# Kernel optimization log

Measured on AMD Instinct MI355X. Metric: run time of the kernel, lower is better.

## Reference

```python
import jax, jax.numpy as jnp
import numpy as np

FORGET_RADIX = 10
HIDDEN_RADIX = 23
LN2 = float(np.log(2.0))
MAX_FORGET = 0.875
BATCH, IN_SIZE, H_SIZE = 8192, 1024, 2048
G = H_SIZE // 2  # group size (h_size // 2)


def setup_inputs() -> dict:
    key = jax.random.key(0)
    ks = jax.random.split(key, 6)
    x = jax.random.normal(ks[0], (BATCH, IN_SIZE), dtype=jnp.float32)
    # hidden is a fixed-point (radix 23) int state; values correspond to floats in (-0.125, 0.125)
    hidden = jax.random.randint(ks[1], (BATCH, H_SIZE), -(2**20), 2**20, dtype=jnp.int32)

    def lin(k, fan_in, fan_out):
        kw, kb = jax.random.split(k)
        s = 1.0 / np.sqrt(fan_in)
        W = jax.random.uniform(kw, (fan_in, fan_out), jnp.float32, -s, s)
        b = jax.random.uniform(kb, (fan_out,), jnp.float32, -s, s)
        return W, b

    W_zr1, b_zr1 = lin(ks[2], IN_SIZE + G, H_SIZE)
    W_g1, b_g1 = lin(ks[3], IN_SIZE + G, G)
    W_zr2, b_zr2 = lin(ks[4], IN_SIZE + G, H_SIZE)
    W_g2, b_g2 = lin(ks[5], IN_SIZE + G, G)
    return {"x": x, "hidden": hidden,
            "W_zr1": W_zr1, "b_zr1": b_zr1, "W_g1": W_g1, "b_g1": b_g1,
            "W_zr2": W_zr2, "b_zr2": b_zr2, "W_g2": W_g2, "b_g2": b_g2,
            "slice_dim": 0}


def _to_float(h_fix, radix):
    # ConvertToFloat: fixed-point int -> float
    return h_fix.astype(jnp.float32) / np.float32(2.0 ** radix)


def _to_fixed(v, radix):
    # ConvertToFixed: float -> fixed-point int (truncation toward zero, like Tensor.int())
    return jnp.trunc(v * np.float32(2.0 ** radix)).astype(jnp.int64)


def reference(x, hidden, W_zr1, b_zr1, W_g1, b_g1, W_zr2, b_zr2, W_g2, b_g2, slice_dim):
    h = hidden.astype(jnp.int64)  # widen so h * z_fix (up to ~2^34) does not overflow
    h1, h2 = h[:, :G], h[:, G:]

    # ---- group 1 update (reads h2) ----
    h2_fl = _to_float(h2, HIDDEN_RADIX)
    zr1 = jax.nn.sigmoid(jnp.concatenate([x, h2_fl], axis=1) @ W_zr1 + b_zr1)
    z1, r1 = zr1[:, :G], zr1[:, G:]
    z1 = MAX_FORGET * z1 + (1.0 - MAX_FORGET)
    g1 = jnp.tanh(jnp.concatenate([x, r1 * h2_fl], axis=1) @ W_g1 + b_g1)
    z1_fix = jnp.maximum(_to_fixed(z1, FORGET_RADIX), 1)  # EnsureNotForgetAll
    h1 = jnp.floor_divide(h1 * z1_fix, 2 ** FORGET_RADIX)  # FixedMultiply, buf=None, mask=1
    h1 = h1 + _to_fixed((1.0 - z1) * g1, HIDDEN_RADIX)     # + MaskFixedMultiply(update1, 1)

    # ---- group 2 update (reads updated h1) ----
    h1_fl = _to_float(h1, HIDDEN_RADIX)
    zr2 = jax.nn.sigmoid(jnp.concatenate([x, h1_fl], axis=1) @ W_zr2 + b_zr2)
    z2, r2 = zr2[:, :G], zr2[:, G:]
    z2 = MAX_FORGET * z2 + (1.0 - MAX_FORGET)
    g2 = jnp.tanh(jnp.concatenate([x, r2 * h1_fl], axis=1) @ W_g2 + b_g2)
    z2_fix = jnp.maximum(_to_fixed(z2, FORGET_RADIX), 1)
    h2 = jnp.floor_divide(h2 * z2_fix, 2 ** FORGET_RADIX)
    h2 = h2 + _to_fixed((1.0 - z2) * g2, HIDDEN_RADIX)

    recurrent_hidden = jnp.concatenate([h1, h2], axis=1).astype(jnp.int32)
    output_hidden = recurrent_hidden.astype(jnp.float32) / np.float32(2.0 ** HIDDEN_RADIX)

    optimal_bits = (jnp.sum(-jnp.log(z1[:, slice_dim:]) / LN2)
                    + jnp.sum(-jnp.log(z2) / LN2)
                    + 32.0 * slice_dim * x.shape[0])
    return recurrent_hidden, output_hidden, optimal_bits
```

## Files before the change

### kernel.cpp

```cpp
#include <hip/hip_runtime.h>
#include <hip/hip_bf16.h>

#define BATCH   8192
#define IN_SZ   1024
#define HSZ     2048
#define GG      1024
#define KTOT    2048

typedef __hip_bfloat16 bf16;
typedef __attribute__((ext_vector_type(8))) short  short8;
typedef __attribute__((ext_vector_type(4))) short  short4e;
typedef __attribute__((ext_vector_type(4))) float  floatx4;

typedef __attribute__((address_space(1))) const void gvoid_t;
typedef __attribute__((address_space(3))) void       lvoid_t;

__device__ __forceinline__ void async_ld16(void* lds, const void* g) {
  __builtin_amdgcn_global_load_lds((gvoid_t*)g, (lvoid_t*)lds, 16, 0, 0);
}

__global__ void prep_all(const float* __restrict__ x, bf16* __restrict__ xb,
                         const int* __restrict__ hidden, bf16* __restrict__ hf,
                         float* accp,
                         const float* __restrict__ W_zr1, const float* __restrict__ W_g1,
                         const float* __restrict__ W_zr2, const float* __restrict__ W_g2,
                         bf16* __restrict__ wt_zr1, bf16* __restrict__ wt_g1,
                         bf16* __restrict__ wt_zr2, bf16* __restrict__ wt_g2) {
  int b = blockIdx.x;
  int t = threadIdx.x;
  if (b < 3072) {
    const float* W; bf16* Wt; int N; int tb = b;
    if (tb < 1024)      { W = W_zr1; Wt = wt_zr1; N = 2048; }
    else if (tb < 1536) { W = W_g1;  Wt = wt_g1;  N = 1024; tb -= 1024; }
    else if (tb < 2560) { W = W_zr2; Wt = wt_zr2; N = 2048; tb -= 1536; }
    else                { W = W_g2;  Wt = wt_g2;  N = 1024; tb -= 2560; }
    int ntn = N >> 6;
    int k0 = (tb / ntn) * 64, n0 = (tb % ntn) * 64;
    __shared__ float tile[64][65];
    int kk = t >> 4, nn = (t & 15) * 4;
#pragma unroll
    for (int s = 0; s < 4; ++s) {
      int row = kk + s * 16;
      float4 v = *(const float4*)&W[(size_t)(k0 + row) * N + n0 + nn];
      tile[row][nn + 0] = v.x; tile[row][nn + 1] = v.y;
      tile[row][nn + 2] = v.z; tile[row][nn + 3] = v.w;
    }
    __syncthreads();
    int k8 = (t & 7) * 8;
#pragma unroll
    for (int s = 0; s < 2; ++s) {
      int nl = (t >> 3) + s * 32;
      bf16 vals[8];
#pragma unroll
      for (int u = 0; u < 8; ++u) vals[u] = __float2bfloat16(tile[k8 + u][nl]);
      *(short8*)&Wt[(size_t)(n0 + nl) * KTOT + k0 + k8] = *(short8*)vals;
    }
  } else {
    int idx = (b - 3072) * 256 + t;
    int i = idx * 4;
    float4 xv = *(const float4*)(x + i);
    xb[i + 0] = __float2bfloat16(xv.x);
    xb[i + 1] = __float2bfloat16(xv.y);
    xb[i + 2] = __float2bfloat16(xv.z);
    xb[i + 3] = __float2bfloat16(xv.w);
    int m = i >> 10, j = i & 1023;
    int4 hv = *(const int4*)(hidden + m * HSZ + GG + j);
    const float sc = 1.0f / 8388608.0f;
    hf[i + 0] = __float2bfloat16((float)hv.x * sc);
    hf[i + 1] = __float2bfloat16((float)hv.y * sc);
    hf[i + 2] = __float2bfloat16((float)hv.z * sc);
    hf[i + 3] = __float2bfloat16((float)hv.w * sc);
    if (idx == 0) *accp = 0.0f;
  }
}


#define BAR() asm volatile("s_barrier" ::: "memory")

#define DS_A(buf, qm) do {                                                   \
  _Pragma("unroll") for (int ii = 0; ii < 4; ++ii) {                         \
    const bf16* _ap = As + (buf)*16384 + (wm*128 + (qm)*64 + ii*16 + r16)*64;\
    af[ii][0] = *(const short8*)(const void*)(_ap + pcq0);                   \
    af[ii][1] = *(const short8*)(const void*)(_ap + pcq1);                   \
  } } while (0)

#define DS_B(buf, qn) do {                                                   \
  _Pragma("unroll") for (int jj = 0; jj < NJQ; ++jj) {                       \
    const int _brow = (BN == 256) ? (wn*64 + (qn)*32 + jj*16 + r16)          \
                                  : (wn*32 + (qn)*16 + r16);                 \
    const bf16* _bp = Bs + (buf)*BSTR + _brow*64;                            \
    bfr[jj][0] = *(const short8*)(const void*)(_bp + pcq0);                  \
    bfr[jj][1] = *(const short8*)(const void*)(_bp + pcq1);                  \
  } } while (0)

#define MFMA_Q(qm, qn) do {                                                  \
  _Pragma("unroll") for (int ii = 0; ii < 4; ++ii)                           \
  _Pragma("unroll") for (int jj = 0; jj < NJQ; ++jj) {                       \
    floatx4& _c = acc[(qm)*4 + ii][(qn)*NJQ + jj];                           \
    _c = __builtin_amdgcn_mfma_f32_16x16x32_bf16(af[ii][0], bfr[jj][0], _c, 0, 0, 0); \
    _c = __builtin_amdgcn_mfma_f32_16x16x32_bf16(af[ii][1], bfr[jj][1], _c, 0, 0, 0); \
  } } while (0)

#define STAGE_A(buf, qm, tk) do {                                            \
  const int _t = (tk);                                                       \
  const bf16* _p = (_t < 16 ? A0 : A1);                                      \
  const int _k = ((_t & 15) << 6) + gch8;                                    \
  async_ld16(As + (buf)*16384 + (qm)*4096 + w*512 + lnoff,        _p + a_sro[qm][0] + _k); \
  async_ld16(As + (buf)*16384 + 8192 + (qm)*4096 + w*512 + lnoff, _p + a_sro[qm][1] + _k); \
} while (0)

#define STAGE_B(buf, qn, tk) do {                                            \
  const int _k = ((tk) << 6) + gch8;                                         \
  if constexpr (BN == 256) {                                                 \
    async_ld16(Bs + (buf)*BSTR + ((w>>2)*64 + (qn)*32 + (w&3)*8)*64 + lnoff,       Bt + b_sro[qn][0] + _k); \
    async_ld16(Bs + (buf)*BSTR + (128 + (w>>2)*64 + (qn)*32 + (w&3)*8)*64 + lnoff, Bt + b_sro[qn][1] + _k); \
  } else {                                                                   \
    async_ld16(Bs + (buf)*BSTR + ((w>>1)*32 + (qn)*16 + (w&1)*8)*64 + lnoff,       Bt + b_sro[qn][0] + _k); \
  }                                                                          \
} while (0)

#define PHASE(buf, qm, qn, NEWA, STAGE_STMT, DOVM) do {                      \
  if (NEWA) DS_A(buf, qm);                                                   \
  DS_B(buf, qn);                                                             \
  STAGE_STMT;                                                                \
  BAR();                                                                     \
  asm volatile("s_waitcnt lgkmcnt(0)" ::: "memory");                         \
  __builtin_amdgcn_sched_barrier(0);                                         \
  __builtin_amdgcn_s_setprio(1);                                             \
  MFMA_Q(qm, qn);                                                            \
  __builtin_amdgcn_s_setprio(0);                                             \
  if (DOVM) { if constexpr (BN == 256) asm volatile("s_waitcnt vmcnt(4)" ::: "memory"); \
              else                     asm volatile("s_waitcnt vmcnt(3)" ::: "memory"); } \
  BAR();                                                                     \
} while (0)

template<int BN>
__device__ __forceinline__ void mainloop8(const bf16* __restrict__ A0,
                                          const bf16* __restrict__ A1,
                                          const bf16* __restrict__ Bt,
                                          bf16* As, bf16* Bs,
                                          int m0, int n0,
                                          floatx4 (&acc)[8][BN / 64]) {
  constexpr int NJQ  = BN / 128;
  constexpr int BSTR = BN * 64;
  const int t    = threadIdx.x;
  const int lane = t & 63;
  const int w    = t >> 6;
  const int l3   = lane >> 3;
  const int gch8 = (((lane & 7) ^ l3) << 3);
  const int lnoff = lane << 3;
  const int wm = w & 1, wn = w >> 1;
  const int q = lane >> 4, r16 = lane & 15;
  const int pcq0 = ((q)     ^ (r16 & 7)) << 3;
  const int pcq1 = ((4 + q) ^ (r16 & 7)) << 3;

  int a_sro[2][2], b_sro[2][2];
#pragma unroll
  for (int qm = 0; qm < 2; ++qm)
#pragma unroll
    for (int h = 0; h < 2; ++h)
      a_sro[qm][h] = (m0 + h*128 + qm*64 + w*8 + l3) * 1024;
#pragma unroll
  for (int qn = 0; qn < 2; ++qn) {
    if constexpr (BN == 256) {
#pragma unroll
      for (int h = 0; h < 2; ++h)
        b_sro[qn][h] = (n0 + h*128 + (w>>2)*64 + qn*32 + (w&3)*8 + l3) * KTOT;
    } else {
      b_sro[qn][0] = (n0 + (w>>1)*32 + qn*16 + (w&1)*8 + l3) * KTOT;
      b_sro[qn][1] = 0;
    }
  }

  STAGE_A(0, 0, 0); STAGE_B(0, 0, 0);
  STAGE_A(0, 1, 0); STAGE_B(0, 1, 0);
  STAGE_A(1, 0, 1); STAGE_B(1, 0, 1);
  if constexpr (BN == 256) asm volatile("s_waitcnt vmcnt(4)" ::: "memory");
  else                     asm volatile("s_waitcnt vmcnt(3)" ::: "memory");
  BAR();

#pragma unroll 1
  for (int it = 0; it < KTOT / 128; ++it) {
    const int tO = 2*it + 1;
    const int t2 = (2*it + 2 < KTOT/64) ? (2*it + 2) : (KTOT/64 - 1);
    const int t3 = (2*it + 3 < KTOT/64) ? (2*it + 3) : (KTOT/64 - 1);
    short8 af[4][2];
    short8 bfr[NJQ][2];
    PHASE(0, 0, 0, 1, STAGE_A(1, 1, tO), 0);
    PHASE(0, 0, 1, 0, STAGE_B(1, 1, tO), 0);
    PHASE(0, 1, 0, 1, STAGE_A(0, 0, t2), 0);
    PHASE(0, 1, 1, 0, STAGE_B(0, 0, t2), 1);
    PHASE(1, 0, 0, 1, STAGE_A(0, 1, t2), 0);
    PHASE(1, 0, 1, 0, STAGE_B(0, 1, t2), 0);
    PHASE(1, 1, 0, 1, STAGE_A(1, 0, t3), 0);
    PHASE(1, 1, 1, 0, STAGE_B(1, 0, t3), 1);
  }
  asm volatile("s_waitcnt vmcnt(0)" ::: "memory");
  __syncthreads();
}

__global__ void __launch_bounds__(512, 2)
gemm_zr8(const bf16* __restrict__ xb, const bf16* __restrict__ hfp,
         const bf16* __restrict__ Bt, const float* __restrict__ bias,
         bf16* __restrict__ zbuf, bf16* __restrict__ rh,
         const int* __restrict__ slice_ptr, int use_slice,
         float* __restrict__ accp) {
  __shared__ __attribute__((aligned(16))) char smem[131072];
  bf16* As = (bf16*)smem;
  bf16* Bs = (bf16*)(smem + 65536);
  const int m0 = blockIdx.y * 256;
  const int n0 = blockIdx.x * 256;
  floatx4 acc[8][4];
#pragma unroll
  for (int i = 0; i < 8; ++i)
#pragma unroll
    for (int j = 0; j < 4; ++j) acc[i][j] = (floatx4)0.0f;

  mainloop8<256>(xb, hfp, Bt, As, Bs, m0, n0, acc);

  const int t = threadIdx.x;
  const int lane = t & 63, w = t >> 6;
  const int wm = w & 1, wn = w >> 1;
  const int q = lane >> 4, r16 = lane & 15;
  float* lds_f = (float*)smem;
  const bool zmode = (n0 < GG);
  const int nmin = use_slice ? *slice_ptr : 0;
  float bn[4];
#pragma unroll
  for (int j = 0; j < 4; ++j) bn[j] = bias[n0 + wn*64 + j*16 + r16];
  float lsum = 0.0f;

#pragma unroll
  for (int p = 0; p < 2; ++p) {
#pragma unroll
    for (int i4 = 0; i4 < 4; ++i4)
#pragma unroll
      for (int j = 0; j < 4; ++j) {
        const int n_loc = wn*64 + j*16 + r16;
        const int n = n0 + n_loc;
#pragma unroll
        for (int rr = 0; rr < 4; ++rr) {
          const int lr = wm*64 + i4*16 + q*4 + rr;
          float v = acc[p*4 + i4][j][rr] + bn[j];
          float s = 1.0f / (1.0f + __expf(-v));
          float ov;
          if (zmode) {
            float z = 0.875f * s + 0.125f;
            if (n >= nmin) lsum += -__log2f(z);
            ov = z;
          } else {
            ov = s;
          }
          lds_f[lr*256 + ((((n_loc >> 2) ^ (lr & 7)) << 2) | (n_loc & 3))] = ov;
        }
      }
    __syncthreads();
#pragma unroll
    for (int s2 = 0; s2 < 16; ++s2) {
      const int r = w*16 + s2;
      const int c = lane;
      floatx4 v4 = *(const floatx4*)&lds_f[r*256 + ((c ^ (r & 7)) << 2)];
      const int m = m0 + (r >> 6)*128 + p*64 + (r & 63);
      const int ncol = n0 + c*4;
      if (zmode) {
        bf16 o[4];
#pragma unroll
        for (int e = 0; e < 4; ++e) o[e] = __float2bfloat16(v4[e]);
        *(short4e*)&zbuf[(size_t)m * GG + ncol] = *(short4e*)o;
      } else {
        const int jc = ncol - GG;
        short4e hv = *(const short4e*)&hfp[(size_t)m * GG + jc];
        bf16 o[4];
#pragma unroll
        for (int e = 0; e < 4; ++e) {
          float hfv = __uint_as_float((unsigned)(unsigned short)hv[e] << 16);
          o[e] = __float2bfloat16(v4[e] * hfv);
        }
        *(short4e*)&rh[(size_t)m * GG + jc] = *(short4e*)o;
      }
    }
    __syncthreads();
  }
#pragma unroll
  for (int off = 32; off > 0; off >>= 1) lsum += __shfl_down(lsum, off, 64);
  float* sf = (float*)smem;
  if (lane == 0) sf[w] = lsum;
  __syncthreads();
  if (t == 0)
    atomicAdd(accp, sf[0]+sf[1]+sf[2]+sf[3]+sf[4]+sf[5]+sf[6]+sf[7]);
}

__global__ void __launch_bounds__(512, 2)
gemm_g8(const bf16* __restrict__ xb, const bf16* __restrict__ rh,
        const bf16* __restrict__ Bt, const float* __restrict__ bias,
        const bf16* __restrict__ zbuf, const int* __restrict__ hidden,
        int col_off,
        float* __restrict__ out0, float* __restrict__ out1,
        bf16* __restrict__ hf_out, int write_hf,
        int write_bits, const float* __restrict__ accp,
        const int* __restrict__ slice_ptr, float* __restrict__ out2) {
  __shared__ __attribute__((aligned(16))) char smem[131072];
  bf16* As = (bf16*)smem;
  bf16* Bs = (bf16*)(smem + 65536);
  const int m0 = blockIdx.y * 256;
  const int n0 = blockIdx.x * 128;
  floatx4 acc[8][2];
#pragma unroll
  for (int i = 0; i < 8; ++i)
#pragma unroll
    for (int j = 0; j < 2; ++j) acc[i][j] = (floatx4)0.0f;

  mainloop8<128>(xb, rh, Bt, As, Bs, m0, n0, acc);

  const int t = threadIdx.x;
  const int lane = t & 63, w = t >> 6;
  const int wm = w & 1, wn = w >> 1;
  const int q = lane >> 4, r16 = lane & 15;
  float* lds_f = (float*)smem;
  float bn[2];
#pragma unroll
  for (int j = 0; j < 2; ++j) bn[j] = bias[n0 + wn*32 + j*16 + r16];

#pragma unroll
  for (int i = 0; i < 8; ++i)
#pragma unroll
    for (int j = 0; j < 2; ++j) {
      const int n_loc = wn*32 + j*16 + r16;
#pragma unroll
      for (int rr = 0; rr < 4; ++rr) {
        const int lr = wm*128 + i*16 + q*4 + rr;
        lds_f[lr*128 + ((((n_loc >> 2) ^ (lr & 7)) << 2) | (n_loc & 3))] =
            acc[i][j][rr] + bn[j];
      }
    }
  __syncthreads();
#pragma unroll
  for (int s2 = 0; s2 < 16; ++s2) {
    const int r = w*2 + (lane >> 5) + s2*16;
    const int c = lane & 31;
    floatx4 v4 = *(const floatx4*)&lds_f[r*128 + ((c ^ (r & 7)) << 2)];
    const int m = m0 + r;
    const int ncol = n0 + c*4;
    short4e zb = *(const short4e*)&zbuf[(size_t)m * GG + ncol];
    int4 hd = *(const int4*)&hidden[(size_t)m * HSZ + col_off + ncol];
    const int hvv[4] = {hd.x, hd.y, hd.z, hd.w};
    floatx4 w0, w1;
    bf16 ob[4];
#pragma unroll
    for (int e = 0; e < 4; ++e) {
      float v = v4[e];
      float ex = __expf(2.0f * v);
      float gg = 1.0f - 2.0f / (ex + 1.0f);
      float z = __uint_as_float((unsigned)(unsigned short)zb[e] << 16);
      int zfix = (int)(z * 1024.0f);
      if (zfix < 1) zfix = 1;
      long long h = hvv[e];
      long long hupd = (h * (long long)zfix) >> 10;
      float t2f = (1.0f - z) * gg * 8388608.0f;
      long long f2 = (long long)t2f;
      int hnew = (int)(hupd + f2);
      w0[e] = (float)hnew;
      w1[e] = (float)hnew * (1.0f / 8388608.0f);
      ob[e] = __float2bfloat16(w1[e]);
    }
    const size_t ob_ = (size_t)m * HSZ + col_off + ncol;
    *(floatx4*)&out0[ob_] = w0;
    *(floatx4*)&out1[ob_] = w1;
    if (write_hf) *(short4e*)&hf_out[(size_t)m * GG + ncol] = *(short4e*)ob;
  }
  if (write_bits && blockIdx.x == 0 && blockIdx.y == 0 && t == 0)
    *out2 = *accp + 32.0f * (float)(*slice_ptr) * (float)BATCH;
}

extern "C" void kernel_launch(void* const* d_in, const int* in_sizes, int n_in,
                              void* d_out, int out_size, void* d_ws, size_t ws_size,
                              hipStream_t stream) {
  const float* x      = (const float*)d_in[0];
  const int*   hidden = (const int*)d_in[1];
  const float* W_zr1  = (const float*)d_in[2];
  const float* b_zr1  = (const float*)d_in[3];
  const float* W_g1   = (const float*)d_in[4];
  const float* b_g1   = (const float*)d_in[5];
  const float* W_zr2  = (const float*)d_in[6];
  const float* b_zr2  = (const float*)d_in[7];
  const float* W_g2   = (const float*)d_in[8];
  const float* b_g2   = (const float*)d_in[9];
  const int*   slice  = (const int*)d_in[10];

  char* ws = (char*)d_ws;
  size_t off = 0;
  auto alloc = [&](size_t bytes) -> void* {
    void* p = ws + off;
    off += (bytes + 255) & ~(size_t)255;
    return p;
  };
  bf16* xb     = (bf16*)alloc((size_t)BATCH * IN_SZ * 2);
  bf16* wt_zr1 = (bf16*)alloc((size_t)2048 * 2048 * 2);
  bf16* wt_g1  = (bf16*)alloc((size_t)1024 * 2048 * 2);
  bf16* wt_zr2 = (bf16*)alloc((size_t)2048 * 2048 * 2);
  bf16* wt_g2  = (bf16*)alloc((size_t)1024 * 2048 * 2);
  bf16* hf     = (bf16*)alloc((size_t)BATCH * GG * 2);
  bf16* rh     = (bf16*)alloc((size_t)BATCH * GG * 2);
  bf16* zbuf   = (bf16*)alloc((size_t)BATCH * GG * 2);
  float* accp  = (float*)alloc(256);

  float* out0 = (float*)d_out;
  float* out1 = out0 + (size_t)BATCH * HSZ;
  float* out2 = out0 + 2 * (size_t)BATCH * HSZ;

  prep_all<<<3072 + 8192, 256, 0, stream>>>(x, xb, hidden, hf, accp,
                                            W_zr1, W_g1, W_zr2, W_g2,
                                            wt_zr1, wt_g1, wt_zr2, wt_g2);

  gemm_zr8<<<dim3(8, 32), 512, 0, stream>>>(xb, hf, wt_zr1, b_zr1, zbuf, rh, slice, 1, accp);
  gemm_g8<<<dim3(8, 32), 512, 0, stream>>>(xb, rh, wt_g1, b_g1, zbuf, hidden, 0,
                                           out0, out1, hf, 1, 0, accp, slice, out2);
  gemm_zr8<<<dim3(8, 32), 512, 0, stream>>>(xb, hf, wt_zr2, b_zr2, zbuf, rh, slice, 0, accp);
  gemm_g8<<<dim3(8, 32), 512, 0, stream>>>(xb, rh, wt_g2, b_g2, zbuf, hidden, 1024,
                                           out0, out1, hf, 0, 1, accp, slice, out2);
}
```

Baseline: 528.3 us.

## Double-buffer register fragments and remap g-GEMM warps to a 4x2 layout

Replaces the shared templated main loop with separate zr and g main loops. Each loop ping-pongs A/B register fragments so the LDS reads for the next quarter-tile are issued before the MFMAs of the current one, waiting with partial lgkmcnt instead of draining to zero. The g GEMM also changes its warp tiling from 2x4 to 4x2 with 64-wide N per warp, and its B staging and epilogue indexing change to match. This adds register pressure and depends on tricky hand-tuned vmcnt and lgkmcnt counts, which risks stalls or races if they are wrong.

```diff
diff --git a/kernel.cpp b/kernel.cpp
--- a/kernel.cpp
+++ b/kernel.cpp
@@ -75,83 +75,50 @@
 }
 
 
-#define BAR() asm volatile("s_barrier" ::: "memory")
-
-#define DS_A(buf, qm) do {                                                   \
-  _Pragma("unroll") for (int ii = 0; ii < 4; ++ii) {                         \
-    const bf16* _ap = As + (buf)*16384 + (wm*128 + (qm)*64 + ii*16 + r16)*64;\
-    af[ii][0] = *(const short8*)(const void*)(_ap + pcq0);                   \
-    af[ii][1] = *(const short8*)(const void*)(_ap + pcq1);                   \
-  } } while (0)
-
-#define DS_B(buf, qn) do {                                                   \
-  _Pragma("unroll") for (int jj = 0; jj < NJQ; ++jj) {                       \
-    const int _brow = (BN == 256) ? (wn*64 + (qn)*32 + jj*16 + r16)          \
-                                  : (wn*32 + (qn)*16 + r16);                 \
-    const bf16* _bp = Bs + (buf)*BSTR + _brow*64;                            \
-    bfr[jj][0] = *(const short8*)(const void*)(_bp + pcq0);                  \
-    bfr[jj][1] = *(const short8*)(const void*)(_bp + pcq1);                  \
-  } } while (0)
-
-#define MFMA_Q(qm, qn) do {                                                  \
-  _Pragma("unroll") for (int ii = 0; ii < 4; ++ii)                           \
-  _Pragma("unroll") for (int jj = 0; jj < NJQ; ++jj) {                       \
-    floatx4& _c = acc[(qm)*4 + ii][(qn)*NJQ + jj];                           \
-    _c = __builtin_amdgcn_mfma_f32_16x16x32_bf16(af[ii][0], bfr[jj][0], _c, 0, 0, 0); \
-    _c = __builtin_amdgcn_mfma_f32_16x16x32_bf16(af[ii][1], bfr[jj][1], _c, 0, 0, 0); \
-  } } while (0)
-
-#define STAGE_A(buf, qm, tk) do {                                            \
-  const int _t = (tk);                                                       \
-  const bf16* _p = (_t < 16 ? A0 : A1);                                      \
-  const int _k = ((_t & 15) << 6) + gch8;                                    \
-  async_ld16(As + (buf)*16384 + (qm)*4096 + w*512 + lnoff,        _p + a_sro[qm][0] + _k); \
-  async_ld16(As + (buf)*16384 + 8192 + (qm)*4096 + w*512 + lnoff, _p + a_sro[qm][1] + _k); \
-} while (0)
-
-#define STAGE_B(buf, qn, tk) do {                                            \
-  const int _k = ((tk) << 6) + gch8;                                         \
-  if constexpr (BN == 256) {                                                 \
-    async_ld16(Bs + (buf)*BSTR + ((w>>2)*64 + (qn)*32 + (w&3)*8)*64 + lnoff,       Bt + b_sro[qn][0] + _k); \
-    async_ld16(Bs + (buf)*BSTR + (128 + (w>>2)*64 + (qn)*32 + (w&3)*8)*64 + lnoff, Bt + b_sro[qn][1] + _k); \
-  } else {                                                                   \
-    async_ld16(Bs + (buf)*BSTR + ((w>>1)*32 + (qn)*16 + (w&1)*8)*64 + lnoff,       Bt + b_sro[qn][0] + _k); \
-  }                                                                          \
-} while (0)
-
-#define PHASE(buf, qm, qn, NEWA, STAGE_STMT, DOVM) do {                      \
-  if (NEWA) DS_A(buf, qm);                                                   \
-  DS_B(buf, qn);                                                             \
-  STAGE_STMT;                                                                \
-  BAR();                                                                     \
-  asm volatile("s_waitcnt lgkmcnt(0)" ::: "memory");                         \
-  __builtin_amdgcn_sched_barrier(0);                                         \
-  __builtin_amdgcn_s_setprio(1);                                             \
-  MFMA_Q(qm, qn);                                                            \
-  __builtin_amdgcn_s_setprio(0);                                             \
-  if (DOVM) { if constexpr (BN == 256) asm volatile("s_waitcnt vmcnt(4)" ::: "memory"); \
-              else                     asm volatile("s_waitcnt vmcnt(3)" ::: "memory"); } \
-  BAR();                                                                     \
-} while (0)
-
-template<int BN>
-__device__ __forceinline__ void mainloop8(const bf16* __restrict__ A0,
-                                          const bf16* __restrict__ A1,
-                                          const bf16* __restrict__ Bt,
-                                          bf16* As, bf16* Bs,
-                                          int m0, int n0,
-                                          floatx4 (&acc)[8][BN / 64]) {
-  constexpr int NJQ  = BN / 128;
-  constexpr int BSTR = BN * 64;
-  const int t    = threadIdx.x;
-  const int lane = t & 63;
-  const int w    = t >> 6;
-  const int l3   = lane >> 3;
+#define BAR()        asm volatile("s_barrier" ::: "memory")
+#define WAIT_VM(n)   asm volatile("s_waitcnt vmcnt(" #n ")" ::: "memory")
+#define WAIT_LG(n)   asm volatile("s_waitcnt lgkmcnt(" #n ")" ::: "memory")
+#define SCHED0       __builtin_amdgcn_sched_barrier(0)
+#define PRIO1        __builtin_amdgcn_s_setprio(1)
+#define PRIO0        __builtin_amdgcn_s_setprio(0)
+
+#define ZR_SA(buf, qm, tk) { const int _kt = (tk) * 64; const bf16* _p; int _kl; \
+  if (_kt < IN_SZ) { _p = A0g; _kl = _kt; } else { _p = A1g; _kl = _kt - IN_SZ; } \
+  async_ld16(As + (buf)*16384 + (qm)*4096 + w*512 + lnoff,        _p + a_sro[qm][0] + _kl + gch8); \
+  async_ld16(As + (buf)*16384 + 8192 + (qm)*4096 + w*512 + lnoff, _p + a_sro[qm][1] + _kl + gch8); }
+
+#define ZR_SB(buf, qn, tk) { const int _k = (tk) * 64 + gch8; \
+  async_ld16(Bs + (buf)*16384 + ((w>>2)*64 + (qn)*32 + (w&3)*8)*64 + lnoff,       Btg + b_sro[qn][0] + _k); \
+  async_ld16(Bs + (buf)*16384 + (128 + (w>>2)*64 + (qn)*32 + (w&3)*8)*64 + lnoff, Btg + b_sro[qn][1] + _k); }
+
+#define ZR_RDA(dst, buf, qm) { _Pragma("unroll") for (int ii = 0; ii < 4; ++ii) { \
+  const bf16* _ap = As + (buf)*16384 + (wm*128 + (qm)*64 + ii*16 + r16)*64; \
+  dst[ii][0] = *(const short8*)(const void*)(_ap + pcq0); \
+  dst[ii][1] = *(const short8*)(const void*)(_ap + pcq1); } }
+
+#define ZR_RDB(dst, buf, qn) { _Pragma("unroll") for (int jj = 0; jj < 2; ++jj) { \
+  const bf16* _bp = Bs + (buf)*16384 + (wn*64 + (qn)*32 + jj*16 + r16)*64; \
+  dst[jj][0] = *(const short8*)(const void*)(_bp + pcq0); \
+  dst[jj][1] = *(const short8*)(const void*)(_bp + pcq1); } }
+
+#define ZR_MF(qm, qn, AF, BF) { _Pragma("unroll") for (int ii = 0; ii < 4; ++ii) \
+  _Pragma("unroll") for (int jj = 0; jj < 2; ++jj) { \
+    floatx4& _c = acc[(qm)*4 + ii][(qn)*2 + jj]; \
+    _c = __builtin_amdgcn_mfma_f32_16x16x32_bf16(AF[ii][0], BF[jj][0], _c, 0, 0, 0); \
+    _c = __builtin_amdgcn_mfma_f32_16x16x32_bf16(AF[ii][1], BF[jj][1], _c, 0, 0, 0); } }
+
+__device__ __forceinline__ void mainloop_zr(const bf16* __restrict__ A0g,
+                                            const bf16* __restrict__ A1g,
+                                            const bf16* __restrict__ Btg,
+                                            bf16* As, bf16* Bs,
+                                            int m0, int n0, floatx4 (&acc)[8][4]) {
+  const int t = threadIdx.x, lane = t & 63, w = t >> 6;
+  const int l3 = lane >> 3;
   const int gch8 = (((lane & 7) ^ l3) << 3);
   const int lnoff = lane << 3;
   const int wm = w & 1, wn = w >> 1;
   const int q = lane >> 4, r16 = lane & 15;
-  const int pcq0 = ((q)     ^ (r16 & 7)) << 3;
+  const int pcq0 = ((q) ^ (r16 & 7)) << 3;
   const int pcq1 = ((4 + q) ^ (r16 & 7)) << 3;
 
   int a_sro[2][2], b_sro[2][2];
@@ -159,41 +126,109 @@
   for (int qm = 0; qm < 2; ++qm)
 #pragma unroll
     for (int h = 0; h < 2; ++h)
-      a_sro[qm][h] = (m0 + h*128 + qm*64 + w*8 + l3) * 1024;
-#pragma unroll
-  for (int qn = 0; qn < 2; ++qn) {
-    if constexpr (BN == 256) {
-#pragma unroll
-      for (int h = 0; h < 2; ++h)
-        b_sro[qn][h] = (n0 + h*128 + (w>>2)*64 + qn*32 + (w&3)*8 + l3) * KTOT;
-    } else {
-      b_sro[qn][0] = (n0 + (w>>1)*32 + qn*16 + (w&1)*8 + l3) * KTOT;
-      b_sro[qn][1] = 0;
-    }
-  }
-
-  STAGE_A(0, 0, 0); STAGE_B(0, 0, 0);
-  STAGE_A(0, 1, 0); STAGE_B(0, 1, 0);
-  STAGE_A(1, 0, 1); STAGE_B(1, 0, 1);
-  if constexpr (BN == 256) asm volatile("s_waitcnt vmcnt(4)" ::: "memory");
-  else                     asm volatile("s_waitcnt vmcnt(3)" ::: "memory");
+      a_sro[qm][h] = (m0 + h*128 + qm*64 + w*8 + l3) * IN_SZ;
+#pragma unroll
+  for (int qn = 0; qn < 2; ++qn)
+#pragma unroll
+    for (int h = 0; h < 2; ++h)
+      b_sro[qn][h] = (n0 + h*128 + (w>>2)*64 + qn*32 + (w&3)*8 + l3) * KTOT;
+
+  short8 afA[4][2], afB[4][2], bfrA[2][2], bfrB[2][2];
+
+  ZR_SA(0,0,0); ZR_SB(0,0,0); ZR_SB(0,1,0); ZR_SA(0,1,0);
+  ZR_SA(1,0,1); ZR_SB(1,0,1); ZR_SB(1,1,1); ZR_SA(1,1,1);
+  WAIT_VM(10);
+  BAR();
+  ZR_RDA(afA, 0, 0);
+  ZR_RDB(bfrA, 0, 0);
+  WAIT_LG(0);
   BAR();
 
 #pragma unroll 1
   for (int it = 0; it < KTOT / 128; ++it) {
-    const int tO = 2*it + 1;
-    const int t2 = (2*it + 2 < KTOT/64) ? (2*it + 2) : (KTOT/64 - 1);
-    const int t3 = (2*it + 3 < KTOT/64) ? (2*it + 3) : (KTOT/64 - 1);
-    short8 af[4][2];
-    short8 bfr[NJQ][2];
-    PHASE(0, 0, 0, 1, STAGE_A(1, 1, tO), 0);
-    PHASE(0, 0, 1, 0, STAGE_B(1, 1, tO), 0);
-    PHASE(0, 1, 0, 1, STAGE_A(0, 0, t2), 0);
-    PHASE(0, 1, 1, 0, STAGE_B(0, 0, t2), 1);
-    PHASE(1, 0, 0, 1, STAGE_A(0, 1, t2), 0);
-    PHASE(1, 0, 1, 0, STAGE_B(0, 1, t2), 0);
-    PHASE(1, 1, 0, 1, STAGE_A(1, 0, t3), 0);
-    PHASE(1, 1, 1, 0, STAGE_B(1, 0, t3), 1);
+    const int tn0 = (2*it + 2 < KTOT/64) ? (2*it + 2) : (KTOT/64 - 1);
+    const int tn1 = (2*it + 3 < KTOT/64) ? (2*it + 3) : (KTOT/64 - 1);
+    ZR_RDB(bfrB,0,1); ZR_SA(0,0,tn0); BAR(); WAIT_LG(4);  SCHED0; PRIO1; ZR_MF(0,0,afA,bfrA); PRIO0; WAIT_VM(10); BAR();
+    ZR_RDA(afB,0,1);  ZR_SB(0,0,tn0); BAR(); WAIT_LG(8);  SCHED0; PRIO1; ZR_MF(0,1,afA,bfrB); PRIO0; WAIT_VM(10); BAR();
+    ZR_RDA(afA,1,0);  ZR_SB(0,1,tn0); BAR(); WAIT_LG(8);  SCHED0; PRIO1; ZR_MF(1,0,afB,bfrA); PRIO0; WAIT_VM(10); BAR();
+    ZR_RDB(bfrA,1,0); ZR_SA(0,1,tn0); BAR(); WAIT_LG(4);  SCHED0; PRIO1; ZR_MF(1,1,afB,bfrB); PRIO0; WAIT_VM(10); BAR();
+    ZR_RDB(bfrB,1,1); ZR_SA(1,0,tn1); BAR(); WAIT_LG(4);  SCHED0; PRIO1; ZR_MF(0,0,afA,bfrA); PRIO0; WAIT_VM(10); BAR();
+    ZR_RDA(afB,1,1);  ZR_SB(1,0,tn1); BAR(); WAIT_LG(8);  SCHED0; PRIO1; ZR_MF(0,1,afA,bfrB); PRIO0; WAIT_VM(10); BAR();
+    ZR_RDA(afA,0,0);  ZR_SB(1,1,tn1); BAR(); WAIT_LG(8);  SCHED0; PRIO1; ZR_MF(1,0,afB,bfrA); PRIO0; WAIT_VM(10); BAR();
+    ZR_RDB(bfrA,0,0); ZR_SA(1,1,tn1); BAR(); WAIT_LG(4);  SCHED0; PRIO1; ZR_MF(1,1,afB,bfrB); PRIO0; WAIT_VM(10); BAR();
+  }
+  asm volatile("s_waitcnt vmcnt(0)" ::: "memory");
+  __syncthreads();
+}
+
+#define G_SB(buf, tk) { const int _k = (tk) * 64 + gch8; \
+  async_ld16(Bs + (buf)*8192 + w*512 + lnoff,        Btg + b_srg[0] + _k); \
+  async_ld16(Bs + (buf)*8192 + 4096 + w*512 + lnoff, Btg + b_srg[1] + _k); }
+
+#define G_RDA(dst, buf, qm) { _Pragma("unroll") for (int ii = 0; ii < 2; ++ii) { \
+  const bf16* _ap = As + (buf)*16384 + (mwb + (qm)*64 + ii*16 + r16)*64; \
+  dst[ii][0] = *(const short8*)(const void*)(_ap + pcq0); \
+  dst[ii][1] = *(const short8*)(const void*)(_ap + pcq1); } }
+
+#define G_RDB(dst, buf, qn) { _Pragma("unroll") for (int jj = 0; jj < 2; ++jj) { \
+  const bf16* _bp = Bs + (buf)*8192 + (nw*64 + (qn)*32 + jj*16 + r16)*64; \
+  dst[jj][0] = *(const short8*)(const void*)(_bp + pcq0); \
+  dst[jj][1] = *(const short8*)(const void*)(_bp + pcq1); } }
+
+#define G_MF(qm, qn, AF, BF) { _Pragma("unroll") for (int ii = 0; ii < 2; ++ii) \
+  _Pragma("unroll") for (int jj = 0; jj < 2; ++jj) { \
+    floatx4& _c = acc[(qm)*2 + ii][(qn)*2 + jj]; \
+    _c = __builtin_amdgcn_mfma_f32_16x16x32_bf16(AF[ii][0], BF[jj][0], _c, 0, 0, 0); \
+    _c = __builtin_amdgcn_mfma_f32_16x16x32_bf16(AF[ii][1], BF[jj][1], _c, 0, 0, 0); } }
+
+__device__ __forceinline__ void mainloop_g(const bf16* __restrict__ A0g,
+                                           const bf16* __restrict__ A1g,
+                                           const bf16* __restrict__ Btg,
+                                           bf16* As, bf16* Bs,
+                                           int m0, int n0, floatx4 (&acc)[4][4]) {
+  const int t = threadIdx.x, lane = t & 63, w = t >> 6;
+  const int l3 = lane >> 3;
+  const int gch8 = (((lane & 7) ^ l3) << 3);
+  const int lnoff = lane << 3;
+  const int mw = w & 3, nw = w >> 2;
+  const int q = lane >> 4, r16 = lane & 15;
+  const int pcq0 = ((q) ^ (r16 & 7)) << 3;
+  const int pcq1 = ((4 + q) ^ (r16 & 7)) << 3;
+  const int mwb = (mw & 1) * 128 + (mw >> 1) * 32;
+
+  int a_sro[2][2], b_srg[2];
+#pragma unroll
+  for (int qm = 0; qm < 2; ++qm)
+#pragma unroll
+    for (int h = 0; h < 2; ++h)
+      a_sro[qm][h] = (m0 + h*128 + qm*64 + w*8 + l3) * IN_SZ;
+#pragma unroll
+  for (int h = 0; h < 2; ++h)
+    b_srg[h] = (n0 + h*64 + w*8 + l3) * KTOT;
+
+  short8 afA[2][2], afB[2][2], bfrA[2][2], bfrB[2][2];
+
+  ZR_SA(0,0,0); G_SB(0,0); ZR_SA(0,1,0);
+  ZR_SA(1,0,1); G_SB(1,1); ZR_SA(1,1,1);
+  WAIT_VM(8);
+  BAR();
+  G_RDA(afA, 0, 0);
+  G_RDB(bfrA, 0, 0);
+  WAIT_LG(0);
+  BAR();
+
+#pragma unroll 1
+  for (int it = 0; it < KTOT / 128; ++it) {
+    const int tn0 = (2*it + 2 < KTOT/64) ? (2*it + 2) : (KTOT/64 - 1);
+    const int tn1 = (2*it + 3 < KTOT/64) ? (2*it + 3) : (KTOT/64 - 1);
+    G_RDB(bfrB,0,1); ZR_SA(0,0,tn0); BAR(); WAIT_LG(4); SCHED0; PRIO1; G_MF(0,0,afA,bfrA); PRIO0; WAIT_VM(8); BAR();
+    G_RDA(afB,0,1);                  BAR(); WAIT_LG(4); SCHED0; PRIO1; G_MF(0,1,afA,bfrB); PRIO0; WAIT_VM(6); BAR();
+    G_RDA(afA,1,0);  G_SB(0,tn0);    BAR(); WAIT_LG(4); SCHED0; PRIO1; G_MF(1,0,afB,bfrA); PRIO0; WAIT_VM(6); BAR();
+    G_RDB(bfrA,1,0); ZR_SA(0,1,tn0); BAR(); WAIT_LG(4); SCHED0; PRIO1; G_MF(1,1,afB,bfrB); PRIO0; WAIT_VM(8); BAR();
+    G_RDB(bfrB,1,1); ZR_SA(1,0,tn1); BAR(); WAIT_LG(4); SCHED0; PRIO1; G_MF(0,0,afA,bfrA); PRIO0; WAIT_VM(8); BAR();
+    G_RDA(afB,1,1);  G_SB(1,tn1);    BAR(); WAIT_LG(4); SCHED0; PRIO1; G_MF(0,1,afA,bfrB); PRIO0; WAIT_VM(8); BAR();
+    G_RDA(afA,0,0);  ZR_SA(1,1,tn1); BAR(); WAIT_LG(4); SCHED0; PRIO1; G_MF(1,0,afB,bfrA); PRIO0; WAIT_VM(8); BAR();
+    G_RDB(bfrA,0,0);                 BAR(); WAIT_LG(4); SCHED0; PRIO1; G_MF(1,1,afB,bfrB); PRIO0; WAIT_VM(8); BAR();
   }
   asm volatile("s_waitcnt vmcnt(0)" ::: "memory");
   __syncthreads();
@@ -216,7 +251,7 @@
 #pragma unroll
     for (int j = 0; j < 4; ++j) acc[i][j] = (floatx4)0.0f;
 
-  mainloop8<256>(xb, hfp, Bt, As, Bs, m0, n0, acc);
+  mainloop_zr(xb, hfp, Bt, As, Bs, m0, n0, acc);
 
   const int t = threadIdx.x;
   const int lane = t & 63, w = t >> 6;
@@ -304,35 +339,42 @@
   bf16* Bs = (bf16*)(smem + 65536);
   const int m0 = blockIdx.y * 256;
   const int n0 = blockIdx.x * 128;
-  floatx4 acc[8][2];
-#pragma unroll
-  for (int i = 0; i < 8; ++i)
-#pragma unroll
-    for (int j = 0; j < 2; ++j) acc[i][j] = (floatx4)0.0f;
-
-  mainloop8<128>(xb, rh, Bt, As, Bs, m0, n0, acc);
+  floatx4 acc[4][4];
+#pragma unroll
+  for (int i = 0; i < 4; ++i)
+#pragma unroll
+    for (int j = 0; j < 4; ++j) acc[i][j] = (floatx4)0.0f;
+
+  mainloop_g(xb, rh, Bt, As, Bs, m0, n0, acc);
 
   const int t = threadIdx.x;
   const int lane = t & 63, w = t >> 6;
-  const int wm = w & 1, wn = w >> 1;
+  const int mw = w & 3, nw = w >> 2;
   const int q = lane >> 4, r16 = lane & 15;
+  const int mwb = (mw & 1) * 128 + (mw >> 1) * 32;
   float* lds_f = (float*)smem;
-  float bn[2];
-#pragma unroll
-  for (int j = 0; j < 2; ++j) bn[j] = bias[n0 + wn*32 + j*16 + r16];
-
-#pragma unroll
-  for (int i = 0; i < 8; ++i)
-#pragma unroll
-    for (int j = 0; j < 2; ++j) {
-      const int n_loc = wn*32 + j*16 + r16;
-#pragma unroll
-      for (int rr = 0; rr < 4; ++rr) {
-        const int lr = wm*128 + i*16 + q*4 + rr;
-        lds_f[lr*128 + ((((n_loc >> 2) ^ (lr & 7)) << 2) | (n_loc & 3))] =
-            acc[i][j][rr] + bn[j];
-      }
-    }
+  float bn[4];
+#pragma unroll
+  for (int qn = 0; qn < 2; ++qn)
+#pragma unroll
+    for (int j = 0; j < 2; ++j) bn[qn*2 + j] = bias[n0 + nw*64 + qn*32 + j*16 + r16];
+
+#pragma unroll
+  for (int qm = 0; qm < 2; ++qm)
+#pragma unroll
+    for (int i = 0; i < 2; ++i)
+#pragma unroll
+      for (int qn = 0; qn < 2; ++qn)
+#pragma unroll
+        for (int j = 0; j < 2; ++j) {
+          const int n_loc = nw*64 + qn*32 + j*16 + r16;
+#pragma unroll
+          for (int rr = 0; rr < 4; ++rr) {
+            const int lr = mwb + qm*64 + i*16 + q*4 + rr;
+            lds_f[lr*128 + ((((n_loc >> 2) ^ (lr & 7)) << 2) | (n_loc & 3))] =
+                acc[qm*2 + i][qn*2 + j][rr] + bn[qn*2 + j];
+          }
+        }
   __syncthreads();
 #pragma unroll
   for (int s2 = 0; s2 < 16; ++s2) {
```

Result: slower. 673.8 us (+27.5%).
